# Optimization experiments

Hardware: AMD Instinct MI355X
Metric: run time of the kernel (lower is better)

## Reference

```python
import jax, jax.numpy as jnp
import numpy as np

EPS = 1e-8
SCALE = 23.0
LEAKY_SLOPE = 0.01  # torch nn.LeakyReLU default

M, B, D = 65536, 2048, 13
H1, H2, H3 = 300, 600, 100


def _linear_params(key, out_f, in_f):
    # torch nn.Linear default init: U(-1/sqrt(in), 1/sqrt(in))
    k1, k2 = jax.random.split(key)
    bound = 1.0 / np.sqrt(in_f)
    W = jax.random.uniform(k1, (out_f, in_f), jnp.float32, -bound, bound)
    b = jax.random.uniform(k2, (out_f,), jnp.float32, -bound, bound)
    return W, b


def setup_inputs() -> dict:
    key = jax.random.key(0)
    ks = jax.random.split(key, 6)
    memory = jax.random.normal(ks[0], (M, D), jnp.float32)
    value = jax.random.normal(ks[1], (B, D), jnp.float32)
    W1, b1 = _linear_params(ks[2], H1, D)
    W2, b2 = _linear_params(ks[3], H2, H1)
    W3, b3 = _linear_params(ks[4], H3, H2)
    W4, b4 = _linear_params(ks[5], D, H3)
    return {"memory": memory, "value": value,
            "W1": W1, "b1": b1, "W2": W2, "b2": b2,
            "W3": W3, "b3": b3, "W4": W4, "b4": b4}


def _mlp(x, W1, b1, W2, b2, W3, b3, W4, b4):
    h = jax.nn.relu(x @ W1.T + b1)                      # [M, 300]
    h = jax.nn.leaky_relu(h @ W2.T + b2, LEAKY_SLOPE)   # [M, 600]
    h = jax.nn.relu(h @ W3.T + b3)                      # [M, 100]
    return jax.nn.leaky_relu(h @ W4.T + b4, LEAKY_SLOPE)  # [M, 13]


def reference(memory, value, W1, b1, W2, b2, W3, b3, W4, b4):
    # abstract_memory = self.net(self.memory)
    t1 = _mlp(memory, W1, b1, W2, b2, W3, b3, W4, b4)   # [M, 13]
    t2 = value.reshape(value.shape[0], -1)              # flatten(value, 1) -> [B, 13]
    # cosine similarity with torch eps clamping on each norm
    t1n = t1 / jnp.maximum(jnp.linalg.norm(t1, axis=-1, keepdims=True), EPS)
    t2n = t2 / jnp.maximum(jnp.linalg.norm(t2, axis=-1, keepdims=True), EPS)
    s = (t2n @ t1n.T) * SCALE                           # [B, M], replaces per-row python loop
    return jnp.max(s, axis=1)                           # [B]
```

## Files before the change

kernel.cpp:

```cpp
#include <hip/hip_runtime.h>


typedef __bf16 bf16x8 __attribute__((ext_vector_type(8)));
typedef float f32x16 __attribute__((ext_vector_type(16)));

constexpr size_t OFF_W1B = 0;
constexpr size_t OFF_W2B = 10240;
constexpr size_t OFF_W3B = 419840;
constexpr size_t OFF_W4B = 583680;
constexpr size_t OFF_T2N = 591872;
constexpr size_t OFF_T1N = 722944;
constexpr size_t OFF_PART= 4917248;

__device__ __forceinline__ bf16x8 ld8(const __bf16* p) {
    return *reinterpret_cast<const bf16x8*>(p);
}
__device__ __forceinline__ f32x16 mfma32(bf16x8 a, bf16x8 b, f32x16 c) {
    return __builtin_amdgcn_mfma_f32_32x32x16_bf16(a, b, c, 0, 0, 0);
}

__device__ __forceinline__ void cvtswap(const f32x16& a, bf16x8& f0, bf16x8& f1) {
    unsigned w[8];
    #pragma unroll
    for (int j = 0; j < 8; j++)
        asm("v_cvt_pk_bf16_f32 %0, %1, %2" : "=v"(w[j]) : "v"(a[2*j]), "v"(a[2*j+1]));
    unsigned a0 = w[0], b0 = w[2]; asm("v_permlane32_swap_b32 %0, %1" : "+v"(a0), "+v"(b0));
    unsigned a1 = w[1], b1 = w[3]; asm("v_permlane32_swap_b32 %0, %1" : "+v"(a1), "+v"(b1));
    unsigned a2 = w[4], b2 = w[6]; asm("v_permlane32_swap_b32 %0, %1" : "+v"(a2), "+v"(b2));
    unsigned a3 = w[5], b3 = w[7]; asm("v_permlane32_swap_b32 %0, %1" : "+v"(a3), "+v"(b3));
    union { unsigned u[4]; bf16x8 v; } p, q;
    p.u[0] = a0; p.u[1] = a1; p.u[2] = b0; p.u[3] = b1; f0 = p.v;
    q.u[0] = a2; q.u[1] = a3; q.u[2] = b2; q.u[3] = b3; f1 = q.v;
}

__global__ void prep_kernel(const float* __restrict__ W1, const float* __restrict__ b1,
                            const float* __restrict__ W2, const float* __restrict__ b2,
                            const float* __restrict__ W3, const float* __restrict__ b3,
                            const float* __restrict__ W4, const float* __restrict__ b4,
                            const float* __restrict__ value, char* __restrict__ ws) {
    __bf16* W1B = (__bf16*)(ws + OFF_W1B);
    __bf16* W2B = (__bf16*)(ws + OFF_W2B);
    __bf16* W3B = (__bf16*)(ws + OFF_W3B);
    __bf16* W4B = (__bf16*)(ws + OFF_W4B);
    __bf16* T2N = (__bf16*)(ws + OFF_T2N);

    int idx = blockIdx.x * 256 + threadIdx.x;
    if (idx < 5120) {
        int e = idx & 7, lane = (idx >> 3) & 63, nt = idx >> 9;
        int n = nt*32 + (lane & 31);
        int k = (lane >> 5)*8 + e;
        float v = 0.0f;
        if (n < 300)      v = (k < 13) ? W1[n*13 + k] : (k == 13 ? b1[n] : 0.0f);
        else if (n == 300) v = (k == 13) ? 1.0f : 0.0f;
        W1B[idx] = (__bf16)v;
        return;
    }
    idx -= 5120;
    if (idx < 204800) {
        int e = idx & 7, lane = (idx >> 3) & 63, r = idx >> 9;
        int ks = r % 20, nt = r / 20;
        int n = nt*32 + (lane & 31);
        int k = ks*16 + (lane >> 5)*8 + e;
        float v = 0.0f;
        if (n < 600)      v = (k < 300) ? W2[n*300 + k] : (k == 300 ? b2[n] : 0.0f);
        else if (n == 600) v = (k == 300) ? 1.0f : 0.0f;
        W2B[idx] = (__bf16)v;
        return;
    }
    idx -= 204800;
    if (idx < 81920) {
        int e = idx & 7, lane = (idx >> 3) & 63, r = idx >> 9;
        int ks = r % 40, nt = r / 40;
        int n = nt*32 + (lane & 31);
        int k = ks*16 + (lane >> 5)*8 + e;
        float v = 0.0f;
        if (n < 100)      v = (k < 600) ? W3[n*600 + k] : (k == 600 ? b3[n] : 0.0f);
        else if (n == 100) v = (k == 600) ? 1.0f : 0.0f;
        W3B[idx] = (__bf16)v;
        return;
    }
    idx -= 81920;
    if (idx < 4096) {
        int e = idx & 7, lane = (idx >> 3) & 63, ks = idx >> 9;
        int n = lane & 31;
        int k = ks*16 + (lane >> 5)*8 + e;
        float v = 0.0f;
        if (n < 13) v = (k < 100) ? W4[n*100 + k] : (k == 100 ? b4[n] : 0.0f);
        W4B[idx] = (__bf16)v;
        return;
    }
    idx -= 4096;
    if (idx < 2048) {
        float v[13]; float s = 0.0f;
        #pragma unroll
        for (int k = 0; k < 13; k++) { v[k] = value[idx*13 + k]; s += v[k]*v[k]; }
        float inv = 1.0f / fmaxf(sqrtf(s), 1e-8f);
        #pragma unroll
        for (int k = 0; k < 13; k++) T2N[idx*32 + k] = (__bf16)(v[k] * inv);
        #pragma unroll
        for (int k = 13; k < 32; k++) T2N[idx*32 + k] = (__bf16)0.0f;
    }
}

__global__ __launch_bounds__(512, 1) void mlp_kernel(const float* __restrict__ mem,
                                                     char* __restrict__ ws) {
    __shared__ char smem[70656];
    __bf16* stg = (__bf16*)smem;
    float*  t1s = (float*)(smem + 57344);

    const __bf16* W1B = (const __bf16*)(ws + OFF_W1B);
    const __bf16* W2B = (const __bf16*)(ws + OFF_W2B);
    const __bf16* W3B = (const __bf16*)(ws + OFF_W3B);
    const __bf16* W4B = (const __bf16*)(ws + OFF_W4B);
    __bf16* T1N = (__bf16*)(ws + OFF_T1N);

    const int tid = threadIdx.x;
    const int wave = tid >> 6, lane = tid & 63;
    const int l31 = lane & 31, hi = lane >> 5;
    const int bm0 = blockIdx.x * 256;
    const int m = bm0 + wave*32 + l31;

    auto src_of = [&](int nt2, int blk) -> const __bf16* {
        return (blk < 20)
            ? W2B + (size_t)(nt2*20 + blk)*512
            : W3B + (size_t)((((blk-20)>>1)*40) + 2*nt2 + ((blk-20)&1))*512;
    };

    bf16x8 sreg[4];
    #pragma unroll
    for (int i = 0; i < 4; i++) {
        const int blk = wave + i*8;
        if (blk < 28) sreg[i] = ld8(src_of(0, blk) + lane*8);
    }

    bf16x8 xf;
    {
        union { __bf16 h[8]; bf16x8 v; } u;
        const float* xr = mem + (size_t)m*13;
        if (hi == 0) {
            #pragma unroll
            for (int e = 0; e < 8; e++) u.h[e] = (__bf16)xr[e];
        } else {
            #pragma unroll
            for (int e = 0; e < 5; e++) u.h[e] = (__bf16)xr[8 + e];
            u.h[5] = (__bf16)1.0f;
            u.h[6] = (__bf16)0.0f;
            u.h[7] = (__bf16)0.0f;
        }
        xf = u.v;
    }

    bf16x8 afc[20];
    #pragma unroll
    for (int nt = 0; nt < 10; nt++) {
        bf16x8 wf = ld8(W1B + (size_t)nt*512 + lane*8);
        f32x16 z = {};
        f32x16 a = mfma32(wf, xf, z);
        #pragma unroll
        for (int r = 0; r < 16; r++) a[r] = fmaxf(a[r], 0.0f);
        cvtswap(a, afc[2*nt], afc[2*nt + 1]);
    }

    #pragma unroll
    for (int i = 0; i < 4; i++) {
        const int blk = wave + i*8;
        if (blk < 28) *reinterpret_cast<bf16x8*>(stg + blk*512 + lane*8) = sreg[i];
    }
    __syncthreads();

    f32x16 acc3[4] = {};
    int buf = 0;
    for (int nt2 = 0; nt2 < 20; nt2++) {
        if (nt2 < 19) {
            #pragma unroll
            for (int i = 0; i < 4; i++) {
                const int blk = wave + i*8;
                if (blk < 28) sreg[i] = ld8(src_of(nt2 + 1, blk) + lane*8);
            }
        }
        const __bf16* sb = stg + buf*14336;
        f32x16 e0 = {}, e1 = {};
        #pragma unroll
        for (int ks = 0; ks < 20; ks += 2) {
            e0 = mfma32(ld8(sb + ks*512 + lane*8),       afc[ks],     e0);
            e1 = mfma32(ld8(sb + (ks + 1)*512 + lane*8), afc[ks + 1], e1);
        }
        #pragma unroll
        for (int r = 0; r < 16; r++) {
            float v = e0[r] + e1[r];
            e0[r] = fmaxf(v, 0.0f) + 0.01f*fminf(v, 0.0f);
        }
        bf16x8 h2f0, h2f1;
        cvtswap(e0, h2f0, h2f1);
        #pragma unroll
        for (int n3 = 0; n3 < 4; n3++) {
            acc3[n3] = mfma32(ld8(sb + (20 + 2*n3)*512 + lane*8), h2f0, acc3[n3]);
            acc3[n3] = mfma32(ld8(sb + (21 + 2*n3)*512 + lane*8), h2f1, acc3[n3]);
        }
        if (nt2 < 19) {
            #pragma unroll
            for (int i = 0; i < 4; i++) {
                const int blk = wave + i*8;
                if (blk < 28)
                    *reinterpret_cast<bf16x8*>(stg + (buf^1)*14336 + blk*512 + lane*8) = sreg[i];
            }
        }
        __syncthreads();
        buf ^= 1;
    }

    f32x16 acc4 = {};
    #pragma unroll
    for (int n3 = 0; n3 < 4; n3++) {
        f32x16 h;
        #pragma unroll
        for (int r = 0; r < 16; r++) h[r] = fmaxf(acc3[n3][r], 0.0f);
        bf16x8 f0, f1;
        cvtswap(h, f0, f1);
        acc4 = mfma32(ld8(W4B + (size_t)(2*n3)*512 + lane*8),     f0, acc4);
        acc4 = mfma32(ld8(W4B + (size_t)(2*n3 + 1)*512 + lane*8), f1, acc4);
    }
    const int mrow = wave*32 + l31;
    #pragma unroll
    for (int r = 0; r < 16; r++) {
        const int n4 = (r & 3) + 8*(r >> 2) + 4*hi;
        if (n4 < 13) {
            float v = acc4[r];
            t1s[mrow*13 + n4] = fmaxf(v, 0.0f) + 0.01f*fminf(v, 0.0f);
        }
    }
    __syncthreads();

    if (tid < 256) {
        float s = 0.0f, v[13];
        #pragma unroll
        for (int k = 0; k < 13; k++) { v[k] = t1s[tid*13 + k]; s += v[k]*v[k]; }
        const float inv = 1.0f / fmaxf(sqrtf(s), 1e-8f);
        __bf16 o[32];
        #pragma unroll
        for (int k = 0; k < 13; k++) o[k] = (__bf16)(v[k] * inv);
        #pragma unroll
        for (int k = 13; k < 32; k++) o[k] = (__bf16)0.0f;
        bf16x8* dst = reinterpret_cast<bf16x8*>(T1N + (size_t)(bm0 + tid)*32);
        const bf16x8* src = reinterpret_cast<const bf16x8*>(o);
        #pragma unroll
        for (int i = 0; i < 4; i++) dst[i] = src[i];
    }
}

__global__ __launch_bounds__(256) void sim_kernel(const char* __restrict__ ws_c,
                                                  float* __restrict__ part) {
    const char* ws = ws_c;
    const __bf16* T1N = (const __bf16*)(ws + OFF_T1N);
    const __bf16* T2N = (const __bf16*)(ws + OFF_T2N);
    const int wave = threadIdx.x >> 6, lane = threadIdx.x & 63;
    const int l31 = lane & 31, l5 = lane >> 5;
    const int bgroup = blockIdx.x & 15, ms = blockIdx.x >> 4;
    const int b0 = (bgroup*4 + wave) * 32;

    const bf16x8 af0 = ld8(T2N + (b0 + l31)*32 + l5*8);
    const bf16x8 af1 = ld8(T2N + (b0 + l31)*32 + 16 + l5*8);
    const f32x16 zero = {};
    f32x16 mx;
    #pragma unroll
    for (int r = 0; r < 16; r++) mx[r] = -3.0e38f;

    #pragma unroll 4
    for (int mt = ms; mt < 2048; mt += 128) {
        const __bf16* p0 = T1N + ((size_t)mt*32 + l31)*32 + l5*8;
        const __bf16* p1 = T1N + ((size_t)(mt + 64)*32 + l31)*32 + l5*8;
        bf16x8 b00 = ld8(p0);
        bf16x8 b01 = ld8(p0 + 16);
        bf16x8 b10 = ld8(p1);
        bf16x8 b11 = ld8(p1 + 16);
        f32x16 d0 = mfma32(af1, b01, mfma32(af0, b00, zero));
        f32x16 d1 = mfma32(af1, b11, mfma32(af0, b10, zero));
        #pragma unroll
        for (int r = 0; r < 16; r++)
            mx[r] = fmaxf(mx[r], fmaxf(d0[r], d1[r]));
    }
    #pragma unroll
    for (int off = 1; off <= 16; off <<= 1) {
        #pragma unroll
        for (int r = 0; r < 16; r++) mx[r] = fmaxf(mx[r], __shfl_xor(mx[r], off));
    }
    if (l31 == 0) {
        #pragma unroll
        for (int reg = 0; reg < 16; reg++)
            part[ms*2048 + b0 + (reg & 3) + 8*(reg >> 2) + 4*l5] = mx[reg];
    }
}

__global__ void reduce_kernel(const float* __restrict__ part, float* __restrict__ out) {
    int b = blockIdx.x*256 + threadIdx.x;
    if (b < 2048) {
        float m = part[b];
        #pragma unroll
        for (int ms = 1; ms < 64; ms++) m = fmaxf(m, part[ms*2048 + b]);
        out[b] = 23.0f * m;
    }
}

extern "C" void kernel_launch(void* const* d_in, const int* in_sizes, int n_in,
                              void* d_out, int out_size, void* d_ws, size_t ws_size,
                              hipStream_t stream) {
    const float* memory = (const float*)d_in[0];
    const float* value  = (const float*)d_in[1];
    const float* W1 = (const float*)d_in[2]; const float* b1 = (const float*)d_in[3];
    const float* W2 = (const float*)d_in[4]; const float* b2 = (const float*)d_in[5];
    const float* W3 = (const float*)d_in[6]; const float* b3 = (const float*)d_in[7];
    const float* W4 = (const float*)d_in[8]; const float* b4 = (const float*)d_in[9];
    char* ws = (char*)d_ws;
    float* part = (float*)(ws + OFF_PART);
    float* out = (float*)d_out;

    prep_kernel<<<1164, 256, 0, stream>>>(W1, b1, W2, b2, W3, b3, W4, b4, value, ws);
    mlp_kernel<<<256, 512, 0, stream>>>(memory, ws);
    sim_kernel<<<1024, 256, 0, stream>>>(ws, part);
    reduce_kernel<<<8, 256, 0, stream>>>(part, out);
}
```

Before: 132.4 us.

## Halve MLP block size, read W3 from global, shrink normalized vectors to K=16

The MLP kernel moves from 512-thread blocks of 256 rows to 256-thread blocks of 128 rows, with two blocks per CU. W3 fragments are now read straight from global/L2 instead of being staged in shared memory, which shrinks the LDS footprint. The normalized t1/t2 vectors are padded to 16 instead of 32 bf16, so the similarity kernel issues one MFMA per tile instead of two and reads half the bytes. The trade-offs are more W2 staging traffic per row processed and uncached-in-LDS W3 loads sitting in the inner loop.

```diff
diff --git a/kernel.cpp b/kernel.cpp
--- a/kernel.cpp
+++ b/kernel.cpp
@@ -9,8 +9,8 @@
 constexpr size_t OFF_W3B = 419840;
 constexpr size_t OFF_W4B = 583680;
 constexpr size_t OFF_T2N = 591872;
-constexpr size_t OFF_T1N = 722944;
-constexpr size_t OFF_PART= 4917248;
+constexpr size_t OFF_T1N = 657408;
+constexpr size_t OFF_PART= 2754560;
 
 __device__ __forceinline__ bf16x8 ld8(const __bf16* p) {
     return *reinterpret_cast<const bf16x8*>(p);
@@ -50,7 +50,7 @@
         int n = nt*32 + (lane & 31);
         int k = (lane >> 5)*8 + e;
         float v = 0.0f;
-        if (n < 300)      v = (k < 13) ? W1[n*13 + k] : (k == 13 ? b1[n] : 0.0f);
+        if (n < 300)       v = (k < 13) ? W1[n*13 + k] : (k == 13 ? b1[n] : 0.0f);
         else if (n == 300) v = (k == 13) ? 1.0f : 0.0f;
         W1B[idx] = (__bf16)v;
         return;
@@ -62,7 +62,7 @@
         int n = nt*32 + (lane & 31);
         int k = ks*16 + (lane >> 5)*8 + e;
         float v = 0.0f;
-        if (n < 600)      v = (k < 300) ? W2[n*300 + k] : (k == 300 ? b2[n] : 0.0f);
+        if (n < 600)       v = (k < 300) ? W2[n*300 + k] : (k == 300 ? b2[n] : 0.0f);
         else if (n == 600) v = (k == 300) ? 1.0f : 0.0f;
         W2B[idx] = (__bf16)v;
         return;
@@ -74,7 +74,7 @@
         int n = nt*32 + (lane & 31);
         int k = ks*16 + (lane >> 5)*8 + e;
         float v = 0.0f;
-        if (n < 100)      v = (k < 600) ? W3[n*600 + k] : (k == 600 ? b3[n] : 0.0f);
+        if (n < 100)       v = (k < 600) ? W3[n*600 + k] : (k == 600 ? b3[n] : 0.0f);
         else if (n == 100) v = (k == 600) ? 1.0f : 0.0f;
         W3B[idx] = (__bf16)v;
         return;
@@ -96,17 +96,17 @@
         for (int k = 0; k < 13; k++) { v[k] = value[idx*13 + k]; s += v[k]*v[k]; }
         float inv = 1.0f / fmaxf(sqrtf(s), 1e-8f);
         #pragma unroll
-        for (int k = 0; k < 13; k++) T2N[idx*32 + k] = (__bf16)(v[k] * inv);
-        #pragma unroll
-        for (int k = 13; k < 32; k++) T2N[idx*32 + k] = (__bf16)0.0f;
-    }
-}
-
-__global__ __launch_bounds__(512, 1) void mlp_kernel(const float* __restrict__ mem,
+        for (int k = 0; k < 13; k++) T2N[idx*16 + k] = (__bf16)(v[k] * inv);
+        #pragma unroll
+        for (int k = 13; k < 16; k++) T2N[idx*16 + k] = (__bf16)0.0f;
+    }
+}
+
+__global__ __launch_bounds__(256, 2) void mlp_kernel(const float* __restrict__ mem,
                                                      char* __restrict__ ws) {
-    __shared__ char smem[70656];
+    __shared__ char smem[47616];
     __bf16* stg = (__bf16*)smem;
-    float*  t1s = (float*)(smem + 57344);
+    float*  t1s = (float*)(smem + 40960);
 
     const __bf16* W1B = (const __bf16*)(ws + OFF_W1B);
     const __bf16* W2B = (const __bf16*)(ws + OFF_W2B);
@@ -117,21 +117,13 @@
     const int tid = threadIdx.x;
     const int wave = tid >> 6, lane = tid & 63;
     const int l31 = lane & 31, hi = lane >> 5;
-    const int bm0 = blockIdx.x * 256;
+    const int bm0 = blockIdx.x * 128;
     const int m = bm0 + wave*32 + l31;
 
-    auto src_of = [&](int nt2, int blk) -> const __bf16* {
-        return (blk < 20)
-            ? W2B + (size_t)(nt2*20 + blk)*512
-            : W3B + (size_t)((((blk-20)>>1)*40) + 2*nt2 + ((blk-20)&1))*512;
-    };
-
-    bf16x8 sreg[4];
-    #pragma unroll
-    for (int i = 0; i < 4; i++) {
-        const int blk = wave + i*8;
-        if (blk < 28) sreg[i] = ld8(src_of(0, blk) + lane*8);
-    }
+    bf16x8 sreg[5];
+    #pragma unroll
+    for (int i = 0; i < 5; i++)
+        sreg[i] = ld8(W2B + (size_t)(tid + i*256)*8);
 
     bf16x8 xf;
     {
@@ -162,10 +154,8 @@
     }
 
     #pragma unroll
-    for (int i = 0; i < 4; i++) {
-        const int blk = wave + i*8;
-        if (blk < 28) *reinterpret_cast<bf16x8*>(stg + blk*512 + lane*8) = sreg[i];
-    }
+    for (int i = 0; i < 5; i++)
+        *reinterpret_cast<bf16x8*>(stg + (tid + i*256)*8) = sreg[i];
     __syncthreads();
 
     f32x16 acc3[4] = {};
@@ -173,12 +163,10 @@
     for (int nt2 = 0; nt2 < 20; nt2++) {
         if (nt2 < 19) {
             #pragma unroll
-            for (int i = 0; i < 4; i++) {
-                const int blk = wave + i*8;
-                if (blk < 28) sreg[i] = ld8(src_of(nt2 + 1, blk) + lane*8);
-            }
-        }
-        const __bf16* sb = stg + buf*14336;
+            for (int i = 0; i < 5; i++)
+                sreg[i] = ld8(W2B + (size_t)(nt2 + 1)*10240 + (size_t)(tid + i*256)*8);
+        }
+        const __bf16* sb = stg + buf*10240;
         f32x16 e0 = {}, e1 = {};
         #pragma unroll
         for (int ks = 0; ks < 20; ks += 2) {
@@ -194,16 +182,14 @@
         cvtswap(e0, h2f0, h2f1);
         #pragma unroll
         for (int n3 = 0; n3 < 4; n3++) {
-            acc3[n3] = mfma32(ld8(sb + (20 + 2*n3)*512 + lane*8), h2f0, acc3[n3]);
-            acc3[n3] = mfma32(ld8(sb + (21 + 2*n3)*512 + lane*8), h2f1, acc3[n3]);
+            const __bf16* bp = W3B + ((size_t)(n3*40 + 2*nt2)*64 + lane)*8;
+            acc3[n3] = mfma32(ld8(bp),       h2f0, acc3[n3]);
+            acc3[n3] = mfma32(ld8(bp + 512), h2f1, acc3[n3]);
         }
         if (nt2 < 19) {
             #pragma unroll
-            for (int i = 0; i < 4; i++) {
-                const int blk = wave + i*8;
-                if (blk < 28)
-                    *reinterpret_cast<bf16x8*>(stg + (buf^1)*14336 + blk*512 + lane*8) = sreg[i];
-            }
+            for (int i = 0; i < 5; i++)
+                *reinterpret_cast<bf16x8*>(stg + (buf^1)*10240 + (tid + i*256)*8) = sreg[i];
         }
         __syncthreads();
         buf ^= 1;
@@ -231,20 +217,19 @@
     }
     __syncthreads();
 
-    if (tid < 256) {
+    if (tid < 128) {
         float s = 0.0f, v[13];
         #pragma unroll
         for (int k = 0; k < 13; k++) { v[k] = t1s[tid*13 + k]; s += v[k]*v[k]; }
         const float inv = 1.0f / fmaxf(sqrtf(s), 1e-8f);
-        __bf16 o[32];
-        #pragma unroll
-        for (int k = 0; k < 13; k++) o[k] = (__bf16)(v[k] * inv);
-        #pragma unroll
-        for (int k = 13; k < 32; k++) o[k] = (__bf16)0.0f;
-        bf16x8* dst = reinterpret_cast<bf16x8*>(T1N + (size_t)(bm0 + tid)*32);
-        const bf16x8* src = reinterpret_cast<const bf16x8*>(o);
-        #pragma unroll
-        for (int i = 0; i < 4; i++) dst[i] = src[i];
+        union { __bf16 o[16]; bf16x8 f[2]; } u;
+        #pragma unroll
+        for (int k = 0; k < 13; k++) u.o[k] = (__bf16)(v[k] * inv);
+        #pragma unroll
+        for (int k = 13; k < 16; k++) u.o[k] = (__bf16)0.0f;
+        bf16x8* dst = reinterpret_cast<bf16x8*>(T1N + (size_t)(bm0 + tid)*16);
+        dst[0] = u.f[0];
+        dst[1] = u.f[1];
     }
 }
 
@@ -254,12 +239,11 @@
     const __bf16* T1N = (const __bf16*)(ws + OFF_T1N);
     const __bf16* T2N = (const __bf16*)(ws + OFF_T2N);
     const int wave = threadIdx.x >> 6, lane = threadIdx.x & 63;
-    const int l31 = lane & 31, l5 = lane >> 5;
+    const int l31 = lane & 31, hi = lane >> 5;
     const int bgroup = blockIdx.x & 15, ms = blockIdx.x >> 4;
     const int b0 = (bgroup*4 + wave) * 32;
 
-    const bf16x8 af0 = ld8(T2N + (b0 + l31)*32 + l5*8);
-    const bf16x8 af1 = ld8(T2N + (b0 + l31)*32 + 16 + l5*8);
+    const bf16x8 af = ld8(T2N + (size_t)(b0 + l31)*16 + hi*8);
     const f32x16 zero = {};
     f32x16 mx;
     #pragma unroll
@@ -267,14 +251,10 @@
 
     #pragma unroll 4
     for (int mt = ms; mt < 2048; mt += 128) {
-        const __bf16* p0 = T1N + ((size_t)mt*32 + l31)*32 + l5*8;
-        const __bf16* p1 = T1N + ((size_t)(mt + 64)*32 + l31)*32 + l5*8;
-        bf16x8 b00 = ld8(p0);
-        bf16x8 b01 = ld8(p0 + 16);
-        bf16x8 b10 = ld8(p1);
-        bf16x8 b11 = ld8(p1 + 16);
-        f32x16 d0 = mfma32(af1, b01, mfma32(af0, b00, zero));
-        f32x16 d1 = mfma32(af1, b11, mfma32(af0, b10, zero));
+        bf16x8 bf0 = ld8(T1N + ((size_t)mt*32 + l31)*16 + hi*8);
+        bf16x8 bf1 = ld8(T1N + ((size_t)(mt + 64)*32 + l31)*16 + hi*8);
+        f32x16 d0 = mfma32(af, bf0, zero);
+        f32x16 d1 = mfma32(af, bf1, zero);
         #pragma unroll
         for (int r = 0; r < 16; r++)
             mx[r] = fmaxf(mx[r], fmaxf(d0[r], d1[r]));
@@ -287,7 +267,7 @@
     if (l31 == 0) {
         #pragma unroll
         for (int reg = 0; reg < 16; reg++)
-            part[ms*2048 + b0 + (reg & 3) + 8*(reg >> 2) + 4*l5] = mx[reg];
+            part[ms*2048 + b0 + (reg & 3) + 8*(reg >> 2) + 4*hi] = mx[reg];
     }
 }
 
@@ -315,7 +295,7 @@
     float* out = (float*)d_out;
 
     prep_kernel<<<1164, 256, 0, stream>>>(W1, b1, W2, b2, W3, b3, W4, b4, value, ws);
-    mlp_kernel<<<256, 512, 0, stream>>>(memory, ws);
+    mlp_kernel<<<512, 256, 0, stream>>>(memory, ws);
     sim_kernel<<<1024, 256, 0, stream>>>(ws, part);
     reduce_kernel<<<8, 256, 0, stream>>>(part, out);
 }
```

After: 124.9 us. 1.06x faster.
